# Optimization experiments

Hardware: AMD Instinct MI355X
Metric: run time of the kernel (lower is better)

## Reference

```python
import jax, jax.numpy as jnp
import numpy as np

B, S, H, D = 2, 2048, 16, 64


def setup_inputs() -> dict:
    key = jax.random.key(0)
    kq, kk, kv, km = jax.random.split(key, 4)
    q = jax.random.normal(kq, (B, S, H, D), dtype=jnp.float32)
    k = jax.random.normal(kk, (B, S, H, D), dtype=jnp.float32)
    v = jax.random.normal(kv, (B, S, H, D), dtype=jnp.float32)
    pattern_mask = jax.random.bernoulli(km, 0.1, (S, S))
    return {"q": q, "k": k, "v": v, "pattern_mask": pattern_mask}


def reference(q, k, v, pattern_mask):
    # Faithful math of the torch module: for each query row i, attend only to
    # columns j where pattern_mask[i, j]; softmax over the selected columns
    # per (batch, head); rows with no selected columns produce zeros.
    head_dim = q.shape[-1]
    scale = 1.0 / jnp.sqrt(jnp.asarray(head_dim, dtype=q.dtype))
    # scores: [B, H, S_q, S_k]
    scores = jnp.einsum('bihd,bjhd->bhij', q, k) * scale
    neg = jnp.finfo(scores.dtype).min
    masked = jnp.where(pattern_mask[None, None, :, :], scores, neg)
    attn = jax.nn.softmax(masked, axis=-1)
    # zero out rows with no active columns (softmax over all-masked row is uniform garbage)
    row_has = jnp.any(pattern_mask, axis=-1)  # [S]
    attn = jnp.where(row_has[None, None, :, None], attn, jnp.zeros((), dtype=attn.dtype))
    # output: [B, S, H, D]
    out = jnp.einsum('bhij,bjhd->bihd', attn, v)
    return out
```

## Files before the change

kernel.cpp:

```cpp
#include <hip/hip_runtime.h>
#include <hip/hip_bf16.h>
#include <math.h>

#define SLEN 2048
#define NBATCH 2
#define NH 16
#define DH 64
#define WPR 64
#define NROUND 32
#define IMGB 8192
#define CONVBLK (NBATCH * NH * NROUND)
#define PACKBLK (SLEN * WPR / 256)

typedef __attribute__((ext_vector_type(4))) short short4v;
typedef __attribute__((ext_vector_type(8))) short short8v;
typedef __attribute__((ext_vector_type(4))) float float4v;

typedef __attribute__((address_space(1))) void gas_void;
typedef __attribute__((address_space(3))) void las_void;

__device__ __forceinline__ unsigned short f2bf(float f) {
  unsigned u = __float_as_uint(f);
  u += 0x7fffu + ((u >> 16) & 1u);
  return (unsigned short)(u >> 16);
}

__device__ __forceinline__ float fexp2(float x) {
#if __has_builtin(__builtin_amdgcn_exp2f)
  return __builtin_amdgcn_exp2f(x);
#else
  return __expf(x * 0.6931471805599453f);
#endif
}

__device__ __forceinline__ unsigned pack_bf2(float a, float b) {
  unsigned ua = __float_as_uint(a); ua += 0x7fffu + ((ua >> 16) & 1u);
  unsigned ub = __float_as_uint(b); ub += 0x7fffu + ((ub >> 16) & 1u);
  return __builtin_amdgcn_perm(ub, ua, 0x07060302u);
}

__device__ __forceinline__ unsigned cvtpk(float lo, float hi) {
  unsigned r;
  asm("v_cvt_pk_bf16_f32 %0, %1, %2" : "=v"(r) : "v"(lo), "v"(hi));
  return r;
}

__device__ __forceinline__ unsigned nib4(unsigned w) {
  return ((w * 0x01020408u) >> 24) & 0xFu;
}

__device__ __forceinline__ int kperm(int kp) {
  return (kp & 0x23) | ((kp >> 1) & 0x0C) | ((kp << 2) & 0x10);
}

__global__ __launch_bounds__(256) void prep_kernel(
    const float* __restrict__ kk, const float* __restrict__ vv,
    const void* __restrict__ mask,
    char* __restrict__ kb, char* __restrict__ vb,
    unsigned* __restrict__ packed) {
  const int tid = threadIdx.x;
  if (blockIdx.x >= CONVBLK) {
    const int w = (blockIdx.x - CONVBLK) * 256 + tid;
    const uint4* bp = (const uint4*)((const char*)mask + (size_t)w * 32);
    uint4 x = bp[0], y = bp[1];
    const unsigned orw = (x.x | x.y) | (x.z | x.w) | (y.x | y.y) | (y.z | y.w);
    __shared__ int s0, sm;
    if (tid == 0) { s0 = 0; sm = 0; }
    __syncthreads();
    const int lane0 = ((tid & 63) == 0);
    if (__any((orw & 0x000000ffu) != 0) && lane0) atomicOr(&s0, 1);
    if (__any((orw & 0xffffff00u) != 0) && lane0) atomicOr(&sm, 1);
    __syncthreads();
    unsigned bits;
    if (s0 && sm) {
      bits = nib4(x.x) | (nib4(x.y) << 4) | (nib4(x.z) << 8) | (nib4(x.w) << 12) |
             (nib4(y.x) << 16) | (nib4(y.y) << 20) | (nib4(y.z) << 24) | (nib4(y.w) << 28);
    } else {
      const unsigned* m = (const unsigned*)mask + (size_t)w * 32;
      bits = 0u;
#pragma unroll
      for (int j = 0; j < 32; j++) bits |= (m[j] ? 1u : 0u) << j;
    }
    packed[w] = bits;
    return;
  }
  const int bid = blockIdx.x;
  const int t = bid & 31;
  const int bh = bid >> 5;
  const int b = bh >> 4, h = bh & 15;
  char* kimg = kb + (size_t)bid * IMGB;
  char* vimg = vb + (size_t)bid * IMGB;

  {
    const int r = tid >> 2;
    const int dg = (tid & 3) << 4;
    const float* src = kk + (((size_t)(b * SLEN + t * 64 + r) * NH + h) * DH + dg);
    const int rimg = kperm(r);
    char* rowp = kimg + rimg * 128;
    const int swz = (rimg & 7) << 4;
#pragma unroll
    for (int i = 0; i < 4; i++) {
      float4v x = *(const float4v*)(src + i * 4);
      const int d0 = dg + i * 4;
      const int off = (d0 * 2) ^ swz;
      union { unsigned u[2]; short4v s4; } cv;
      cv.u[0] = pack_bf2(x.x, x.y);
      cv.u[1] = pack_bf2(x.z, x.w);
      *(short4v*)(rowp + off) = cv.s4;
    }
  }
  {
    const int d = tid >> 2;
    const int kg = (tid & 3) << 4;
    char* rowp = vimg + d * 128;
    const int swz = (d & 7) << 4;
    const float* src = vv + ((size_t)(b * SLEN + t * 64 + kg) * NH + h) * DH + d;
#pragma unroll
    for (int i = 0; i < 16; i++) {
      const int c = kg + i;
      float x = src[(size_t)i * (NH * DH)];
      const int off = (c * 2) ^ swz;
      *(unsigned short*)(rowp + off) = f2bf(x);
    }
  }
}

__global__ __launch_bounds__(256, 4) void sattn_fast6(
    const float* __restrict__ q, const unsigned* __restrict__ pmask,
    const char* __restrict__ kb, const char* __restrict__ vb,
    float* __restrict__ out) {
  __shared__ __align__(16) char Kbuf[2][IMGB];
  __shared__ __align__(16) char Vbuf[2][IMGB];

  const int tid = threadIdx.x;
  const int xcd = blockIdx.x & 7;
  const int j = blockIdx.x >> 3;
  const int bh = xcd * 4 + (j >> 5);
  const int chunk = j & 31;
  const int b = bh >> 4;
  const int h = bh & 15;
  const int wave = tid >> 6;
  const int lane = tid & 63;
  const int lq = lane & 15;
  const int g = lane >> 4;
  const int swz = (lq & 7) << 4;
  const int g8 = g << 3;
  const int g16 = g << 4;

  const int qrow = chunk * 64 + wave * 16 + lq;
  const int qw = qrow * WPR;

  const float SCL2 = 0.18033688011112042f;
  short8v qf[2];
  {
    const float* qp = q + (((size_t)b * SLEN + qrow) * NH + h) * DH;
#pragma unroll
    for (int ds = 0; ds < 2; ds++) {
      float4v x0 = *(const float4v*)(qp + ds * 32 + g8);
      float4v x1 = *(const float4v*)(qp + ds * 32 + g8 + 4);
      union { unsigned u[4]; short8v s8; } cv;
      cv.u[0] = pack_bf2(x0.x * SCL2, x0.y * SCL2);
      cv.u[1] = pack_bf2(x0.z * SCL2, x0.w * SCL2);
      cv.u[2] = pack_bf2(x1.x * SCL2, x1.y * SCL2);
      cv.u[3] = pack_bf2(x1.z * SCL2, x1.w * SCL2);
      qf[ds] = cv.s8;
    }
  }

  short8v ones;
#pragma unroll
  for (int i = 0; i < 8; i++) ones[i] = (short)0x3F80;

  const char* gK = kb + (size_t)bh * (NROUND * IMGB) + tid * 16;
  const char* gV = vb + (size_t)bh * (NROUND * IMGB) + tid * 16;

  float4v acc[4] = {};
  float4v lacc = {};

  uint2 m = *(const uint2*)&pmask[qw];

  {
    char* lK = &Kbuf[0][0] + tid * 16;
    char* lV = &Vbuf[0][0] + tid * 16;
#pragma unroll
    for (int i = 0; i < 2; i++) {
      __builtin_amdgcn_global_load_lds((gas_void*)(gK + i * 4096), (las_void*)(lK + i * 4096), 16, 0, 0);
      __builtin_amdgcn_global_load_lds((gas_void*)(gV + i * 4096), (las_void*)(lV + i * 4096), 16, 0, 0);
    }
  }
  __syncthreads();

  for (int t = 0; t < NROUND; t++) {
    const int bt = t & 1;
    const unsigned m0 = m.x, m1 = m.y;
    if (t + 1 < NROUND) {
      m = *(const uint2*)&pmask[qw + 2 * (t + 1)];
      const char* nK = gK + (size_t)(t + 1) * IMGB;
      const char* nV = gV + (size_t)(t + 1) * IMGB;
      char* lK = &Kbuf[bt ^ 1][0] + tid * 16;
      char* lV = &Vbuf[bt ^ 1][0] + tid * 16;
#pragma unroll
      for (int i = 0; i < 2; i++) {
        __builtin_amdgcn_global_load_lds((gas_void*)(nK + i * 4096), (las_void*)(lK + i * 4096), 16, 0, 0);
        __builtin_amdgcn_global_load_lds((gas_void*)(nV + i * 4096), (las_void*)(lV + i * 4096), 16, 0, 0);
      }
    }

    const char* Kl = &Kbuf[bt][0];
    float4v st[4];
    __builtin_amdgcn_s_setprio(1);
#pragma unroll
    for (int s = 0; s < 4; s++) {
      const char* rowp = Kl + (s * 16 + lq) * 128;
      short8v kf0 = *(const short8v*)(rowp + ((g16) ^ swz));
      short8v kf1 = *(const short8v*)(rowp + ((64 + g16) ^ swz));
      float4v z = {0.f, 0.f, 0.f, 0.f};
      z = __builtin_amdgcn_mfma_f32_16x16x32_bf16(kf0, qf[0], z, 0, 0, 0);
      z = __builtin_amdgcn_mfma_f32_16x16x32_bf16(kf1, qf[1], z, 0, 0, 0);
      st[s] = z;
    }
    __builtin_amdgcn_s_setprio(0);

    const char* Vl = &Vbuf[bt][0];
    short8v vf[4][2];
#pragma unroll
    for (int n = 0; n < 4; n++) {
      const char* rowp = Vl + (n * 16 + lq) * 128;
      vf[n][0] = *(const short8v*)(rowp + ((g16) ^ swz));
      vf[n][1] = *(const short8v*)(rowp + ((64 + g16) ^ swz));
    }

    float pv[4][4];
#pragma unroll
    for (int s = 0; s < 4; s++) {
      const int sh = g8 + ((s & 1) << 2);
      const unsigned hw = ((s < 2) ? m0 : m1) >> sh;
      float p0 = fexp2(st[s][0]); p0 = (hw & 1u) ? p0 : 0.f;
      float p1 = fexp2(st[s][1]); p1 = (hw & 2u) ? p1 : 0.f;
      float p2 = fexp2(st[s][2]); p2 = (hw & 4u) ? p2 : 0.f;
      float p3 = fexp2(st[s][3]); p3 = (hw & 8u) ? p3 : 0.f;
      pv[s][0] = p0; pv[s][1] = p1; pv[s][2] = p2; pv[s][3] = p3;
    }
    short8v pf[2];
#pragma unroll
    for (int kt = 0; kt < 2; kt++) {
      union { unsigned u[4]; short8v s8; } pa;
      pa.u[0] = cvtpk(pv[2 * kt][0], pv[2 * kt][1]);
      pa.u[1] = cvtpk(pv[2 * kt][2], pv[2 * kt][3]);
      pa.u[2] = cvtpk(pv[2 * kt + 1][0], pv[2 * kt + 1][1]);
      pa.u[3] = cvtpk(pv[2 * kt + 1][2], pv[2 * kt + 1][3]);
      pf[kt] = pa.s8;
    }

    __builtin_amdgcn_s_setprio(1);
    lacc = __builtin_amdgcn_mfma_f32_16x16x32_bf16(ones, pf[0], lacc, 0, 0, 0);
    lacc = __builtin_amdgcn_mfma_f32_16x16x32_bf16(ones, pf[1], lacc, 0, 0, 0);
#pragma unroll
    for (int n = 0; n < 4; n++) {
      float4v a = acc[n];
      a = __builtin_amdgcn_mfma_f32_16x16x32_bf16(vf[n][0], pf[0], a, 0, 0, 0);
      a = __builtin_amdgcn_mfma_f32_16x16x32_bf16(vf[n][1], pf[1], a, 0, 0, 0);
      acc[n] = a;
    }
    __builtin_amdgcn_s_setprio(0);
    __syncthreads();
  }

  const float l = lacc[0];
  const float inv = (l > 0.f) ? 1.f / l : 0.f;
  float* op = out + (((size_t)b * SLEN + qrow) * NH + h) * DH;
#pragma unroll
  for (int n = 0; n < 4; n++) {
    float4v o;
    o.x = acc[n][0] * inv; o.y = acc[n][1] * inv;
    o.z = acc[n][2] * inv; o.w = acc[n][3] * inv;
    *(float4v*)(op + n * 16 + g * 4) = o;
  }
}

__global__ __launch_bounds__(256) void sattn_fallback(
    const float* __restrict__ q, const float* __restrict__ kk,
    const float* __restrict__ vv, const unsigned int* __restrict__ pmask,
    float* __restrict__ out) {
  __shared__ __align__(16) unsigned short Kt[16 * 64];
  __shared__ __align__(16) unsigned short Vt[64 * 20];

  const int tid = threadIdx.x;
  const int chunk = blockIdx.x & 31;
  const int bh = blockIdx.x >> 5;
  const int b = bh >> 4;
  const int h = bh & 15;
  const int wave = tid >> 6;
  const int lane = tid & 63;
  const int lq = lane & 15;
  const int g = lane >> 4;

  const int qrow = chunk * 64 + wave * 16 + lq;

  short4v qf[4];
  {
    const float* qp = q + (((size_t)b * SLEN + qrow) * NH + h) * DH;
#pragma unroll
    for (int ks = 0; ks < 4; ks++) {
      float4v x = *(const float4v*)(qp + ks * 16 + g * 4);
      short4v s;
      s.x = (short)f2bf(x.x); s.y = (short)f2bf(x.y);
      s.z = (short)f2bf(x.z); s.w = (short)f2bf(x.w);
      qf[ks] = s;
    }
  }

  const int srow = tid >> 4;
  const int scol = (tid & 15) * 4;
  const size_t kvbase = (size_t)b * SLEN * (NH * DH) + (size_t)h * DH;

  float4v acc[4] = {};
  float m_run = -INFINITY;
  float l_run = 0.f;

  for (int t = 0; t < SLEN / 16; t++) {
    const int kbase = t * 16;
    __syncthreads();
    {
      const size_t rowoff = kvbase + (size_t)(kbase + srow) * (NH * DH) + scol;
      float4v x = *(const float4v*)(kk + rowoff);
      short4v s;
      s.x = (short)f2bf(x.x); s.y = (short)f2bf(x.y);
      s.z = (short)f2bf(x.z); s.w = (short)f2bf(x.w);
      const int off = (scol * 2) ^ ((srow & 7) << 4);
      *(short4v*)((char*)Kt + srow * 128 + off) = s;

      float4v y = *(const float4v*)(vv + rowoff);
      Vt[(scol + 0) * 20 + srow] = f2bf(y.x);
      Vt[(scol + 1) * 20 + srow] = f2bf(y.y);
      Vt[(scol + 2) * 20 + srow] = f2bf(y.z);
      Vt[(scol + 3) * 20 + srow] = f2bf(y.w);
    }
    __syncthreads();

    float4v stv = {0.f, 0.f, 0.f, 0.f};
#pragma unroll
    for (int ks = 0; ks < 4; ks++) {
      const int off = ((ks * 16 + g * 4) * 2) ^ ((lq & 7) << 4);
      short4v kf = *(const short4v*)((const char*)Kt + lq * 128 + off);
      stv = __builtin_amdgcn_mfma_f32_16x16x16bf16_1k(kf, qf[ks], stv, 0, 0, 0);
    }

    const unsigned int mw = pmask[qrow * WPR + (kbase >> 5)];
    const int shift = (kbase & 16) + g * 4;
    float sc[4];
    float tmax = -INFINITY;
#pragma unroll
    for (int r = 0; r < 4; r++) {
      bool a = (mw >> (shift + r)) & 1u;
      sc[r] = a ? stv[r] * 0.125f : -INFINITY;
      tmax = fmaxf(tmax, sc[r]);
    }
    tmax = fmaxf(tmax, __shfl_xor(tmax, 16));
    tmax = fmaxf(tmax, __shfl_xor(tmax, 32));
    const float mnew = fmaxf(m_run, tmax);
    const float muse = (mnew > -1e37f) ? mnew : 0.f;
    const float alpha = __expf(m_run - muse);
    float p[4], tsum = 0.f;
#pragma unroll
    for (int r = 0; r < 4; r++) {
      p[r] = __expf(sc[r] - muse);
      tsum += p[r];
    }
    tsum += __shfl_xor(tsum, 16);
    tsum += __shfl_xor(tsum, 32);
    l_run = l_run * alpha + tsum;
    m_run = mnew;

    short4v pfv;
    pfv.x = (short)f2bf(p[0]); pfv.y = (short)f2bf(p[1]);
    pfv.z = (short)f2bf(p[2]); pfv.w = (short)f2bf(p[3]);

#pragma unroll
    for (int n = 0; n < 4; n++) {
      acc[n][0] *= alpha; acc[n][1] *= alpha;
      acc[n][2] *= alpha; acc[n][3] *= alpha;
      short4v vf = *(const short4v*)((const char*)Vt + ((n * 16 + lq) * 20 + g * 4) * 2);
      acc[n] = __builtin_amdgcn_mfma_f32_16x16x16bf16_1k(vf, pfv, acc[n], 0, 0, 0);
    }
  }

  const float inv = (l_run > 0.f) ? 1.f / l_run : 0.f;
  float* op = out + (((size_t)b * SLEN + qrow) * NH + h) * DH;
#pragma unroll
  for (int n = 0; n < 4; n++) {
    float4v o;
    o.x = acc[n][0] * inv; o.y = acc[n][1] * inv;
    o.z = acc[n][2] * inv; o.w = acc[n][3] * inv;
    *(float4v*)(op + n * 16 + g * 4) = o;
  }
}

extern "C" void kernel_launch(void* const* d_in, const int* in_sizes, int n_in,
                              void* d_out, int out_size, void* d_ws, size_t ws_size,
                              hipStream_t stream) {
  const float* q = (const float*)d_in[0];
  const float* k = (const float*)d_in[1];
  const float* v = (const float*)d_in[2];
  const void* mask = d_in[3];
  float* out = (float*)d_out;

  unsigned int* packed = (unsigned int*)((char*)d_ws + 256);
  char* kb = (char*)d_ws + (1 << 20);
  char* vb = kb + (size_t)NBATCH * NH * NROUND * IMGB;
  const size_t need = (size_t)(1 << 20) + 2 * (size_t)NBATCH * NH * NROUND * IMGB;

  prep_kernel<<<CONVBLK + PACKBLK, 256, 0, stream>>>(k, v, mask, kb, vb, packed);
  if (ws_size >= need) {
    sattn_fast6<<<NBATCH * NH * (SLEN / 64), 256, 0, stream>>>(q, packed, kb, vb, out);
  } else {
    sattn_fallback<<<NBATCH * NH * (SLEN / 64), 256, 0, stream>>>(q, k, v, packed, out);
  }
}
```

Before: 77.04 us.

## Switch attention to 32x32x16 MFMA tiles with 128-row query chunks

The main attention kernel moves from 16x16x32 to 32x32x16 bf16 MFMA instructions. Each wave now handles 32 query rows, so a block covers 128 rows, and the grid is halved. The prep kernel permutes V columns to match the new P fragment layout and drops the K row permutation. The goal is to reuse each K/V tile loaded into LDS across twice as many queries, halving LDS and global K/V traffic per query. The cost is more registers (launch bounds lowered to 2 blocks) and fewer blocks to fill the GPU.

```diff
diff --git a/kernel.cpp b/kernel.cpp
--- a/kernel.cpp
+++ b/kernel.cpp
@@ -15,6 +15,7 @@
 typedef __attribute__((ext_vector_type(4))) short short4v;
 typedef __attribute__((ext_vector_type(8))) short short8v;
 typedef __attribute__((ext_vector_type(4))) float float4v;
+typedef __attribute__((ext_vector_type(16))) float float16v;
 
 typedef __attribute__((address_space(1))) void gas_void;
 typedef __attribute__((address_space(3))) void las_void;
@@ -49,8 +50,9 @@
   return ((w * 0x01020408u) >> 24) & 0xFu;
 }
 
-__device__ __forceinline__ int kperm(int kp) {
-  return (kp & 0x23) | ((kp >> 1) & 0x0C) | ((kp << 2) & 0x10);
+__device__ __forceinline__ int vcol(int p) {
+  const int kc = 2 * (p >> 5) + ((p >> 4) & 1);
+  return 16 * kc + 8 * ((p >> 2) & 1) + 4 * ((p >> 3) & 1) + (p & 3);
 }
 
 __global__ __launch_bounds__(256) void prep_kernel(
@@ -95,14 +97,13 @@
     const int r = tid >> 2;
     const int dg = (tid & 3) << 4;
     const float* src = kk + (((size_t)(b * SLEN + t * 64 + r) * NH + h) * DH + dg);
-    const int rimg = kperm(r);
-    char* rowp = kimg + rimg * 128;
-    const int swz = (rimg & 7) << 4;
+    char* rowp = kimg + r * 128;
+    const int swzk = (r & 7) << 4;
 #pragma unroll
     for (int i = 0; i < 4; i++) {
       float4v x = *(const float4v*)(src + i * 4);
       const int d0 = dg + i * 4;
-      const int off = (d0 * 2) ^ swz;
+      const int off = (d0 * 2) ^ swzk;
       union { unsigned u[2]; short4v s4; } cv;
       cv.u[0] = pack_bf2(x.x, x.y);
       cv.u[1] = pack_bf2(x.z, x.w);
@@ -113,19 +114,19 @@
     const int d = tid >> 2;
     const int kg = (tid & 3) << 4;
     char* rowp = vimg + d * 128;
-    const int swz = (d & 7) << 4;
+    const int swzv = (d & 7) << 4;
     const float* src = vv + ((size_t)(b * SLEN + t * 64 + kg) * NH + h) * DH + d;
 #pragma unroll
     for (int i = 0; i < 16; i++) {
-      const int c = kg + i;
+      const int p = kg + i;
       float x = src[(size_t)i * (NH * DH)];
-      const int off = (c * 2) ^ swz;
+      const int off = (vcol(p) * 2) ^ swzv;
       *(unsigned short*)(rowp + off) = f2bf(x);
     }
   }
 }
 
-__global__ __launch_bounds__(256, 4) void sattn_fast6(
+__global__ __launch_bounds__(256, 2) void sattn_fast7(
     const float* __restrict__ q, const unsigned* __restrict__ pmask,
     const char* __restrict__ kb, const char* __restrict__ vb,
     float* __restrict__ out) {
@@ -135,29 +136,27 @@
   const int tid = threadIdx.x;
   const int xcd = blockIdx.x & 7;
   const int j = blockIdx.x >> 3;
-  const int bh = xcd * 4 + (j >> 5);
-  const int chunk = j & 31;
+  const int bh = xcd * 4 + (j >> 4);
+  const int chunk = j & 15;
   const int b = bh >> 4;
-  const int h = bh & 15;
+  const int hd = bh & 15;
   const int wave = tid >> 6;
   const int lane = tid & 63;
-  const int lq = lane & 15;
-  const int g = lane >> 4;
-  const int swz = (lq & 7) << 4;
-  const int g8 = g << 3;
-  const int g16 = g << 4;
-
-  const int qrow = chunk * 64 + wave * 16 + lq;
+  const int l31 = lane & 31;
+  const int hl = lane >> 5;
+  const int swz = (l31 & 7) << 4;
+
+  const int qrow = chunk * 128 + wave * 32 + l31;
   const int qw = qrow * WPR;
 
   const float SCL2 = 0.18033688011112042f;
-  short8v qf[2];
+  short8v qf[4];
   {
-    const float* qp = q + (((size_t)b * SLEN + qrow) * NH + h) * DH;
-#pragma unroll
-    for (int ds = 0; ds < 2; ds++) {
-      float4v x0 = *(const float4v*)(qp + ds * 32 + g8);
-      float4v x1 = *(const float4v*)(qp + ds * 32 + g8 + 4);
+    const float* qp = q + (((size_t)b * SLEN + qrow) * NH + hd) * DH;
+#pragma unroll
+    for (int ds = 0; ds < 4; ds++) {
+      float4v x0 = *(const float4v*)(qp + ds * 16 + hl * 8);
+      float4v x1 = *(const float4v*)(qp + ds * 16 + hl * 8 + 4);
       union { unsigned u[4]; short8v s8; } cv;
       cv.u[0] = pack_bf2(x0.x * SCL2, x0.y * SCL2);
       cv.u[1] = pack_bf2(x0.z * SCL2, x0.w * SCL2);
@@ -174,8 +173,7 @@
   const char* gK = kb + (size_t)bh * (NROUND * IMGB) + tid * 16;
   const char* gV = vb + (size_t)bh * (NROUND * IMGB) + tid * 16;
 
-  float4v acc[4] = {};
-  float4v lacc = {};
+  float16v acc0 = {}, acc1 = {}, lacc = {};
 
   uint2 m = *(const uint2*)&pmask[qw];
 
@@ -207,60 +205,70 @@
     }
 
     const char* Kl = &Kbuf[bt][0];
-    float4v st[4];
+    float16v st0, st1;
     __builtin_amdgcn_s_setprio(1);
-#pragma unroll
-    for (int s = 0; s < 4; s++) {
-      const char* rowp = Kl + (s * 16 + lq) * 128;
-      short8v kf0 = *(const short8v*)(rowp + ((g16) ^ swz));
-      short8v kf1 = *(const short8v*)(rowp + ((64 + g16) ^ swz));
-      float4v z = {0.f, 0.f, 0.f, 0.f};
-      z = __builtin_amdgcn_mfma_f32_16x16x32_bf16(kf0, qf[0], z, 0, 0, 0);
-      z = __builtin_amdgcn_mfma_f32_16x16x32_bf16(kf1, qf[1], z, 0, 0, 0);
-      st[s] = z;
+    {
+      float16v z = {};
+#pragma unroll
+      for (int ds = 0; ds < 4; ds++) {
+        short8v kf = *(const short8v*)(Kl + (l31)*128 + ((ds * 32 + hl * 16) ^ swz));
+        z = __builtin_amdgcn_mfma_f32_32x32x16_bf16(kf, qf[ds], z, 0, 0, 0);
+      }
+      st0 = z;
+    }
+    {
+      float16v z = {};
+#pragma unroll
+      for (int ds = 0; ds < 4; ds++) {
+        short8v kf = *(const short8v*)(Kl + (32 + l31) * 128 + ((ds * 32 + hl * 16) ^ swz));
+        z = __builtin_amdgcn_mfma_f32_32x32x16_bf16(kf, qf[ds], z, 0, 0, 0);
+      }
+      st1 = z;
     }
     __builtin_amdgcn_s_setprio(0);
 
+    float p0[16], p1[16];
+#pragma unroll
+    for (int u = 0; u < 4; u++) {
+      const unsigned hw0 = m0 >> (8 * u + 4 * hl);
+      const unsigned hw1 = m1 >> (8 * u + 4 * hl);
+      {
+        float a0 = fexp2(st0[4 * u + 0]); a0 = (hw0 & 1u) ? a0 : 0.f;
+        float a1 = fexp2(st0[4 * u + 1]); a1 = (hw0 & 2u) ? a1 : 0.f;
+        float a2 = fexp2(st0[4 * u + 2]); a2 = (hw0 & 4u) ? a2 : 0.f;
+        float a3 = fexp2(st0[4 * u + 3]); a3 = (hw0 & 8u) ? a3 : 0.f;
+        p0[4 * u + 0] = a0; p0[4 * u + 1] = a1; p0[4 * u + 2] = a2; p0[4 * u + 3] = a3;
+      }
+      {
+        float a0 = fexp2(st1[4 * u + 0]); a0 = (hw1 & 1u) ? a0 : 0.f;
+        float a1 = fexp2(st1[4 * u + 1]); a1 = (hw1 & 2u) ? a1 : 0.f;
+        float a2 = fexp2(st1[4 * u + 2]); a2 = (hw1 & 4u) ? a2 : 0.f;
+        float a3 = fexp2(st1[4 * u + 3]); a3 = (hw1 & 8u) ? a3 : 0.f;
+        p1[4 * u + 0] = a0; p1[4 * u + 1] = a1; p1[4 * u + 2] = a2; p1[4 * u + 3] = a3;
+      }
+    }
+    short8v pf[4];
+    {
+      union { unsigned u[4]; short8v s8; } c0, c1, c2, c3;
+#pragma unroll
+      for (int jj = 0; jj < 4; jj++) {
+        c0.u[jj] = cvtpk(p0[2 * jj], p0[2 * jj + 1]);
+        c1.u[jj] = cvtpk(p0[8 + 2 * jj], p0[8 + 2 * jj + 1]);
+        c2.u[jj] = cvtpk(p1[2 * jj], p1[2 * jj + 1]);
+        c3.u[jj] = cvtpk(p1[8 + 2 * jj], p1[8 + 2 * jj + 1]);
+      }
+      pf[0] = c0.s8; pf[1] = c1.s8; pf[2] = c2.s8; pf[3] = c3.s8;
+    }
+
     const char* Vl = &Vbuf[bt][0];
-    short8v vf[4][2];
-#pragma unroll
-    for (int n = 0; n < 4; n++) {
-      const char* rowp = Vl + (n * 16 + lq) * 128;
-      vf[n][0] = *(const short8v*)(rowp + ((g16) ^ swz));
-      vf[n][1] = *(const short8v*)(rowp + ((64 + g16) ^ swz));
-    }
-
-    float pv[4][4];
-#pragma unroll
-    for (int s = 0; s < 4; s++) {
-      const int sh = g8 + ((s & 1) << 2);
-      const unsigned hw = ((s < 2) ? m0 : m1) >> sh;
-      float p0 = fexp2(st[s][0]); p0 = (hw & 1u) ? p0 : 0.f;
-      float p1 = fexp2(st[s][1]); p1 = (hw & 2u) ? p1 : 0.f;
-      float p2 = fexp2(st[s][2]); p2 = (hw & 4u) ? p2 : 0.f;
-      float p3 = fexp2(st[s][3]); p3 = (hw & 8u) ? p3 : 0.f;
-      pv[s][0] = p0; pv[s][1] = p1; pv[s][2] = p2; pv[s][3] = p3;
-    }
-    short8v pf[2];
-#pragma unroll
-    for (int kt = 0; kt < 2; kt++) {
-      union { unsigned u[4]; short8v s8; } pa;
-      pa.u[0] = cvtpk(pv[2 * kt][0], pv[2 * kt][1]);
-      pa.u[1] = cvtpk(pv[2 * kt][2], pv[2 * kt][3]);
-      pa.u[2] = cvtpk(pv[2 * kt + 1][0], pv[2 * kt + 1][1]);
-      pa.u[3] = cvtpk(pv[2 * kt + 1][2], pv[2 * kt + 1][3]);
-      pf[kt] = pa.s8;
-    }
-
     __builtin_amdgcn_s_setprio(1);
-    lacc = __builtin_amdgcn_mfma_f32_16x16x32_bf16(ones, pf[0], lacc, 0, 0, 0);
-    lacc = __builtin_amdgcn_mfma_f32_16x16x32_bf16(ones, pf[1], lacc, 0, 0, 0);
-#pragma unroll
-    for (int n = 0; n < 4; n++) {
-      float4v a = acc[n];
-      a = __builtin_amdgcn_mfma_f32_16x16x32_bf16(vf[n][0], pf[0], a, 0, 0, 0);
-      a = __builtin_amdgcn_mfma_f32_16x16x32_bf16(vf[n][1], pf[1], a, 0, 0, 0);
-      acc[n] = a;
+#pragma unroll
+    for (int kc = 0; kc < 4; kc++) {
+      short8v vf0 = *(const short8v*)(Vl + (l31)*128 + ((kc * 32 + hl * 16) ^ swz));
+      acc0 = __builtin_amdgcn_mfma_f32_32x32x16_bf16(vf0, pf[kc], acc0, 0, 0, 0);
+      short8v vf1 = *(const short8v*)(Vl + (32 + l31) * 128 + ((kc * 32 + hl * 16) ^ swz));
+      acc1 = __builtin_amdgcn_mfma_f32_32x32x16_bf16(vf1, pf[kc], acc1, 0, 0, 0);
+      lacc = __builtin_amdgcn_mfma_f32_32x32x16_bf16(ones, pf[kc], lacc, 0, 0, 0);
     }
     __builtin_amdgcn_s_setprio(0);
     __syncthreads();
@@ -268,13 +276,16 @@
 
   const float l = lacc[0];
   const float inv = (l > 0.f) ? 1.f / l : 0.f;
-  float* op = out + (((size_t)b * SLEN + qrow) * NH + h) * DH;
-#pragma unroll
-  for (int n = 0; n < 4; n++) {
-    float4v o;
-    o.x = acc[n][0] * inv; o.y = acc[n][1] * inv;
-    o.z = acc[n][2] * inv; o.w = acc[n][3] * inv;
-    *(float4v*)(op + n * 16 + g * 4) = o;
+  float* op = out + (((size_t)b * SLEN + qrow) * NH + hd) * DH;
+#pragma unroll
+  for (int u = 0; u < 4; u++) {
+    float4v o0, o1;
+    o0.x = acc0[4 * u + 0] * inv; o0.y = acc0[4 * u + 1] * inv;
+    o0.z = acc0[4 * u + 2] * inv; o0.w = acc0[4 * u + 3] * inv;
+    o1.x = acc1[4 * u + 0] * inv; o1.y = acc1[4 * u + 1] * inv;
+    o1.z = acc1[4 * u + 2] * inv; o1.w = acc1[4 * u + 3] * inv;
+    *(float4v*)(op + 8 * u + 4 * hl) = o0;
+    *(float4v*)(op + 32 + 8 * u + 4 * hl) = o1;
   }
 }
 
@@ -412,7 +423,7 @@
 
   prep_kernel<<<CONVBLK + PACKBLK, 256, 0, stream>>>(k, v, mask, kb, vb, packed);
   if (ws_size >= need) {
-    sattn_fast6<<<NBATCH * NH * (SLEN / 64), 256, 0, stream>>>(q, packed, kb, vb, out);
+    sattn_fast7<<<NBATCH * NH * (SLEN / 128), 256, 0, stream>>>(q, packed, kb, vb, out);
   } else {
     sattn_fallback<<<NBATCH * NH * (SLEN / 64), 256, 0, stream>>>(q, k, v, packed, out);
   }
```

Result: slower. 80.54 us (+4.5%).
